# Kernel tuning notes

Hardware: AMD Instinct MI355X
Metric: run time of the kernel (lower is better)

The kernel has to match this reference:

```python
import jax, jax.numpy as jnp
import numpy as np

B, I, H = 2048, 512, 512


def _hamilton_matrix(W):
    """W: [4, O, Iin] quaternion weight components (r,i,j,k).
    Returns real block matrix M: [4*Iin, 4*O] implementing the Hamilton
    product W (*) x for component-major flattened input [r|i|j|k]."""
    Wr, Wi, Wj, Wk = W[0].T, W[1].T, W[2].T, W[3].T  # each [Iin, O]
    row_r = jnp.concatenate([Wr, Wi, Wj, Wk], axis=1)
    row_i = jnp.concatenate([-Wi, Wr, Wk, -Wj], axis=1)
    row_j = jnp.concatenate([-Wj, -Wk, Wr, Wi], axis=1)
    row_k = jnp.concatenate([-Wk, Wj, -Wi, Wr], axis=1)
    return jnp.concatenate([row_r, row_i, row_j, row_k], axis=0)


def qlinear(x, W, b=None):
    """x: [B, Iin, 4]; W: [4, O, Iin]; b: [O, 4] or None -> [B, O, 4]."""
    Bn, Iin, _ = x.shape
    O = W.shape[1]
    xf = x.transpose(0, 2, 1).reshape(Bn, 4 * Iin)  # component-major flatten
    out = xf @ _hamilton_matrix(W)                   # [B, 4*O]
    out = out.reshape(Bn, 4, O).transpose(0, 2, 1)   # [B, O, 4]
    if b is not None:
        out = out + b
    return out


def setup_inputs() -> dict:
    key = jax.random.key(0)
    ks = jax.random.split(key, 16)
    s_in = 0.02   # weight scale for numerical sanity
    d = {
        "x": jax.random.normal(ks[0], (B, I, 4), jnp.float32),
        "h": jax.random.normal(ks[1], (B, H, 4), jnp.float32),
        "c": jax.random.normal(ks[2], (B, H, 4), jnp.float32),
        "Wi_w": jax.random.normal(ks[3], (4, H, I), jnp.float32) * s_in,
        "Wf_w": jax.random.normal(ks[4], (4, H, I), jnp.float32) * s_in,
        "Wo_w": jax.random.normal(ks[5], (4, H, I), jnp.float32) * s_in,
        "Wc_w": jax.random.normal(ks[6], (4, H, I), jnp.float32) * s_in,
        "Ui_w": jax.random.normal(ks[7], (4, H, H), jnp.float32) * s_in,
        "Uf_w": jax.random.normal(ks[8], (4, H, H), jnp.float32) * s_in,
        "Uo_w": jax.random.normal(ks[9], (4, H, H), jnp.float32) * s_in,
        "Uc_w": jax.random.normal(ks[10], (4, H, H), jnp.float32) * s_in,
        "Ui_b": jax.random.normal(ks[11], (H, 4), jnp.float32) * s_in,
        "Uf_b": jax.random.normal(ks[12], (H, 4), jnp.float32) * s_in,
        "Uo_b": jax.random.normal(ks[13], (H, 4), jnp.float32) * s_in,
        "Uc_b": jax.random.normal(ks[14], (H, 4), jnp.float32) * s_in,
    }
    return d


def reference(x, h, c, Wi_w, Wf_w, Wo_w, Wc_w, Ui_w, Uf_w, Uo_w, Uc_w,
              Ui_b, Uf_b, Uo_b, Uc_b):
    # Scalar gates from real (index-0) component of quaternion gate preacts.
    i_pre = qlinear(x, Wi_w) + qlinear(h, Ui_w, Ui_b)
    f_pre = qlinear(x, Wf_w) + qlinear(h, Uf_w, Uf_b)
    o_pre = qlinear(x, Wo_w) + qlinear(h, Uo_w, Uo_b)
    c_tilde = jnp.tanh(qlinear(x, Wc_w) + qlinear(h, Uc_w, Uc_b))
    i = jax.nn.sigmoid(i_pre[..., 0])[..., None]  # [B, H, 1] broadcasts over 4 comps
    f = jax.nn.sigmoid(f_pre[..., 0])[..., None]
    o = jax.nn.sigmoid(o_pre[..., 0])[..., None]
    c_t = f * c + i * c_tilde
    h_t = o * jnp.tanh(c_t)
    return (h_t, c_t)
```

## Files before the change

### kernel.cpp

```cpp
#include <hip/hip_runtime.h>
#include <hip/hip_bf16.h>


#define BDIM 256

typedef __attribute__((ext_vector_type(8))) short short8;
typedef __attribute__((ext_vector_type(4))) float f32x4;

typedef const __attribute__((address_space(1))) void* gptr_t;
typedef __attribute__((address_space(3))) void* lptr_t;

__device__ __forceinline__ ushort f2b(float f) {
  __hip_bfloat16 h = __float2bfloat16(f);
  union { __hip_bfloat16 b; ushort u; } cv;
  cv.b = h;
  return cv.u;
}

__global__ __launch_bounds__(BDIM) void pack_a_kernel(
    const float* __restrict__ x, const float* __restrict__ h,
    ushort* __restrict__ A) {
  int tid = blockIdx.x * BDIM + threadIdx.x;
  int b = tid >> 8;
  int pos0 = (tid & 255) << 2;
  const float* src = (pos0 < 512)
      ? (x + ((size_t)b * 512 + pos0) * 4)
      : (h + ((size_t)b * 512 + (pos0 - 512)) * 4);
  float4 q0 = reinterpret_cast<const float4*>(src)[0];
  float4 q1 = reinterpret_cast<const float4*>(src)[1];
  float4 q2 = reinterpret_cast<const float4*>(src)[2];
  float4 q3 = reinterpret_cast<const float4*>(src)[3];
  ushort* Ab = A + (size_t)b * 4096 + pos0;
  union { ushort u[4]; uint2 v; } r0, r1, r2, r3;
  r0.u[0] = f2b(q0.x); r0.u[1] = f2b(q1.x); r0.u[2] = f2b(q2.x); r0.u[3] = f2b(q3.x);
  r1.u[0] = f2b(q0.y); r1.u[1] = f2b(q1.y); r1.u[2] = f2b(q2.y); r1.u[3] = f2b(q3.y);
  r2.u[0] = f2b(q0.z); r2.u[1] = f2b(q1.z); r2.u[2] = f2b(q2.z); r2.u[3] = f2b(q3.z);
  r3.u[0] = f2b(q0.w); r3.u[1] = f2b(q1.w); r3.u[2] = f2b(q2.w); r3.u[3] = f2b(q3.w);
  *reinterpret_cast<uint2*>(Ab)        = r0.v;
  *reinterpret_cast<uint2*>(Ab + 1024) = r1.v;
  *reinterpret_cast<uint2*>(Ab + 2048) = r2.v;
  *reinterpret_cast<uint2*>(Ab + 3072) = r3.v;
}

__global__ __launch_bounds__(BDIM) void pack_w_kernel(
    const float* __restrict__ w0, const float* __restrict__ w1,
    const float* __restrict__ w2, const float* __restrict__ w3,
    const float* __restrict__ u0, const float* __restrict__ u1,
    const float* __restrict__ u2, const float* __restrict__ u3,
    ushort* __restrict__ Wp) {
  int tid = blockIdx.x * BDIM + threadIdx.x;
  int n = tid >> 9;
  int k = (tid & 511) << 3;
  int blk = n >> 9, o = n & 511;
  int cin = k >> 10, pos = k & 1023;
  int part = pos >> 9, ii = pos & 511;
  int g  = blk < 3 ? blk : 3;
  int co = blk < 3 ? 0 : blk - 3;
  int comp = cin ^ co;
  float sg = ((0x5390u >> ((cin << 2) | co)) & 1u) ? -1.0f : 1.0f;
  const float* base;
  if (part == 0) base = (g == 0) ? w0 : (g == 1) ? w1 : (g == 2) ? w2 : w3;
  else           base = (g == 0) ? u0 : (g == 1) ? u1 : (g == 2) ? u2 : u3;
  const float* p = base + (size_t)comp * 262144 + (size_t)o * 512 + ii;
  float4 v0 = *reinterpret_cast<const float4*>(p);
  float4 v1 = *reinterpret_cast<const float4*>(p + 4);
  union { ushort u[8]; uint4 v; } r;
  r.u[0] = f2b(sg * v0.x); r.u[1] = f2b(sg * v0.y);
  r.u[2] = f2b(sg * v0.z); r.u[3] = f2b(sg * v0.w);
  r.u[4] = f2b(sg * v1.x); r.u[5] = f2b(sg * v1.y);
  r.u[6] = f2b(sg * v1.z); r.u[7] = f2b(sg * v1.w);
  *reinterpret_cast<uint4*>(Wp + (size_t)n * 4096 + k) = r.v;
}

__global__ __launch_bounds__(BDIM, 2) void gemm_kernel(
    const ushort* __restrict__ A, const ushort* __restrict__ Bt,
    float* __restrict__ C) {
  __shared__ ushort As[128 * 32];
  __shared__ ushort Bs[128 * 32];
  const int t = threadIdx.x;
  const int lane = t & 63;
  const int wid = t >> 6;
  const int wm = wid >> 1, wn = wid & 1;
  const int lrow = lane & 15;
  const int lk = (lane >> 4) << 3;
  const int m0 = blockIdx.y * 128;
  const int n0 = blockIdx.x * 128;

  f32x4 acc[4][4];
#pragma unroll
  for (int mi = 0; mi < 4; ++mi)
#pragma unroll
    for (int ni = 0; ni < 4; ++ni)
      acc[mi][ni] = (f32x4){0.f, 0.f, 0.f, 0.f};

  const int rA = t >> 2;
  const int cA = (t & 3) << 3;
  const ushort* Abase = A + (size_t)m0 * 4096;
  const ushort* Bbase = Bt + (size_t)n0 * 4096;

  for (int kt = 0; kt < 4096; kt += 32) {
#pragma unroll
    for (int ch = 0; ch < 2; ++ch) {
      const ushort* ga = Abase + (size_t)(ch * 64 + rA) * 4096 + kt + cA;
      const ushort* gb = Bbase + (size_t)(ch * 64 + rA) * 4096 + kt + cA;
      __builtin_amdgcn_global_load_lds((gptr_t)ga, (lptr_t)(As + ch * 2048 + t * 8),
                                       16, 0, 0);
      __builtin_amdgcn_global_load_lds((gptr_t)gb, (lptr_t)(Bs + ch * 2048 + t * 8),
                                       16, 0, 0);
    }
    __syncthreads();
    short8 a[4], b[4];
#pragma unroll
    for (int f = 0; f < 4; ++f) {
      a[f] = *reinterpret_cast<const short8*>(As + (wm * 64 + f * 16 + lrow) * 32 + lk);
      b[f] = *reinterpret_cast<const short8*>(Bs + (wn * 64 + f * 16 + lrow) * 32 + lk);
    }
#pragma unroll
    for (int mi = 0; mi < 4; ++mi)
#pragma unroll
      for (int ni = 0; ni < 4; ++ni)
        acc[mi][ni] = __builtin_amdgcn_mfma_f32_16x16x32_bf16(
            a[mi], b[ni], acc[mi][ni], 0, 0, 0);
    __syncthreads();
  }

  const int orow = (lane >> 4) << 2;
#pragma unroll
  for (int mi = 0; mi < 4; ++mi) {
#pragma unroll
    for (int ni = 0; ni < 4; ++ni) {
      float* cp = C + (size_t)(m0 + wm * 64 + mi * 16 + orow) * 3584
                  + (n0 + wn * 64 + ni * 16 + (lane & 15));
#pragma unroll
      for (int r = 0; r < 4; ++r)
        cp[(size_t)r * 3584] = acc[mi][ni][r];
    }
  }
}

__global__ __launch_bounds__(BDIM) void cell_kernel(
    const float* __restrict__ pre, const float* __restrict__ cin,
    const float* __restrict__ bi, const float* __restrict__ bfg,
    const float* __restrict__ bo, const float* __restrict__ bc,
    float* __restrict__ out) {
  int tid = blockIdx.x * BDIM + threadIdx.x;
  int o = tid & 511;
  const float* row = pre + (size_t)(tid >> 9) * 3584;
  float4 bcv = *reinterpret_cast<const float4*>(bc + (size_t)o * 4);
  float ip = row[o]        + bi[o << 2];
  float fp = row[512 + o]  + bfg[o << 2];
  float op = row[1024 + o] + bo[o << 2];
  float g0 = tanhf(row[1536 + o] + bcv.x);
  float g1 = tanhf(row[2048 + o] + bcv.y);
  float g2 = tanhf(row[2560 + o] + bcv.z);
  float g3 = tanhf(row[3072 + o] + bcv.w);
  float ig = 1.f / (1.f + expf(-ip));
  float fg = 1.f / (1.f + expf(-fp));
  float og = 1.f / (1.f + expf(-op));
  float4 cv = *reinterpret_cast<const float4*>(cin + (size_t)tid * 4);
  float4 ct, ht;
  ct.x = fg * cv.x + ig * g0;  ht.x = og * tanhf(ct.x);
  ct.y = fg * cv.y + ig * g1;  ht.y = og * tanhf(ct.y);
  ct.z = fg * cv.z + ig * g2;  ht.z = og * tanhf(ct.z);
  ct.w = fg * cv.w + ig * g3;  ht.w = og * tanhf(ct.w);
  *reinterpret_cast<float4*>(out + (size_t)tid * 4) = ht;
  *reinterpret_cast<float4*>(out + 4194304 + (size_t)tid * 4) = ct;
}

extern "C" void kernel_launch(void* const* d_in, const int* in_sizes, int n_in,
                              void* d_out, int out_size, void* d_ws, size_t ws_size,
                              hipStream_t stream) {
  const float* x   = (const float*)d_in[0];
  const float* h   = (const float*)d_in[1];
  const float* c   = (const float*)d_in[2];
  const float* wi  = (const float*)d_in[3];
  const float* wf  = (const float*)d_in[4];
  const float* wo  = (const float*)d_in[5];
  const float* wc  = (const float*)d_in[6];
  const float* ui  = (const float*)d_in[7];
  const float* uf  = (const float*)d_in[8];
  const float* uo  = (const float*)d_in[9];
  const float* uc  = (const float*)d_in[10];
  const float* bi  = (const float*)d_in[11];
  const float* bf_ = (const float*)d_in[12];
  const float* bo  = (const float*)d_in[13];
  const float* bc  = (const float*)d_in[14];
  float* out = (float*)d_out;

  ushort* A  = (ushort*)d_ws;
  ushort* Wp = (ushort*)((char*)d_ws + (size_t)16777216);
  float* pre = (float*)((char*)d_ws + (size_t)16777216 + 29360128);

  hipLaunchKernelGGL(pack_a_kernel, dim3(2048), dim3(BDIM), 0, stream, x, h, A);
  hipLaunchKernelGGL(pack_w_kernel, dim3(7168), dim3(BDIM), 0, stream,
                     wi, wf, wo, wc, ui, uf, uo, uc, Wp);
  hipLaunchKernelGGL(gemm_kernel, dim3(28, 16), dim3(BDIM), 0, stream, A, Wp, pre);
  hipLaunchKernelGGL(cell_kernel, dim3(4096), dim3(BDIM), 0, stream,
                     pre, c, bi, bf_, bo, bc, out);
}
```

Measured before the change: 247.2 us.

## Fuse LSTM cell epilogue into GEMM and merge pack kernels

Merges the activation and weight pack kernels into one launch. It reorders weight columns so each output index owns 8 contiguous columns (7 gates plus one zero pad), which lets the GEMM block compute complete gate sets for 16 outputs. The cell nonlinearity then runs in the GEMM epilogue through a shared-memory staging tile. This removes the round trip of the fp32 preactivation buffer through global memory and two kernel launches. In exchange it adds padding work (3584 to 4096 columns, 32 column blocks instead of 28) and more shared memory per block, which may reduce occupancy.

```diff
diff --git a/kernel.cpp b/kernel.cpp
--- a/kernel.cpp
+++ b/kernel.cpp
@@ -17,66 +17,75 @@
   return cv.u;
 }
 
-__global__ __launch_bounds__(BDIM) void pack_a_kernel(
+__global__ __launch_bounds__(BDIM) void pack_kernel(
     const float* __restrict__ x, const float* __restrict__ h,
-    ushort* __restrict__ A) {
-  int tid = blockIdx.x * BDIM + threadIdx.x;
-  int b = tid >> 8;
-  int pos0 = (tid & 255) << 2;
-  const float* src = (pos0 < 512)
-      ? (x + ((size_t)b * 512 + pos0) * 4)
-      : (h + ((size_t)b * 512 + (pos0 - 512)) * 4);
-  float4 q0 = reinterpret_cast<const float4*>(src)[0];
-  float4 q1 = reinterpret_cast<const float4*>(src)[1];
-  float4 q2 = reinterpret_cast<const float4*>(src)[2];
-  float4 q3 = reinterpret_cast<const float4*>(src)[3];
-  ushort* Ab = A + (size_t)b * 4096 + pos0;
-  union { ushort u[4]; uint2 v; } r0, r1, r2, r3;
-  r0.u[0] = f2b(q0.x); r0.u[1] = f2b(q1.x); r0.u[2] = f2b(q2.x); r0.u[3] = f2b(q3.x);
-  r1.u[0] = f2b(q0.y); r1.u[1] = f2b(q1.y); r1.u[2] = f2b(q2.y); r1.u[3] = f2b(q3.y);
-  r2.u[0] = f2b(q0.z); r2.u[1] = f2b(q1.z); r2.u[2] = f2b(q2.z); r2.u[3] = f2b(q3.z);
-  r3.u[0] = f2b(q0.w); r3.u[1] = f2b(q1.w); r3.u[2] = f2b(q2.w); r3.u[3] = f2b(q3.w);
-  *reinterpret_cast<uint2*>(Ab)        = r0.v;
-  *reinterpret_cast<uint2*>(Ab + 1024) = r1.v;
-  *reinterpret_cast<uint2*>(Ab + 2048) = r2.v;
-  *reinterpret_cast<uint2*>(Ab + 3072) = r3.v;
-}
-
-__global__ __launch_bounds__(BDIM) void pack_w_kernel(
     const float* __restrict__ w0, const float* __restrict__ w1,
     const float* __restrict__ w2, const float* __restrict__ w3,
     const float* __restrict__ u0, const float* __restrict__ u1,
     const float* __restrict__ u2, const float* __restrict__ u3,
-    ushort* __restrict__ Wp) {
-  int tid = blockIdx.x * BDIM + threadIdx.x;
-  int n = tid >> 9;
-  int k = (tid & 511) << 3;
-  int blk = n >> 9, o = n & 511;
-  int cin = k >> 10, pos = k & 1023;
-  int part = pos >> 9, ii = pos & 511;
-  int g  = blk < 3 ? blk : 3;
-  int co = blk < 3 ? 0 : blk - 3;
-  int comp = cin ^ co;
-  float sg = ((0x5390u >> ((cin << 2) | co)) & 1u) ? -1.0f : 1.0f;
-  const float* base;
-  if (part == 0) base = (g == 0) ? w0 : (g == 1) ? w1 : (g == 2) ? w2 : w3;
-  else           base = (g == 0) ? u0 : (g == 1) ? u1 : (g == 2) ? u2 : u3;
-  const float* p = base + (size_t)comp * 262144 + (size_t)o * 512 + ii;
-  float4 v0 = *reinterpret_cast<const float4*>(p);
-  float4 v1 = *reinterpret_cast<const float4*>(p + 4);
-  union { ushort u[8]; uint4 v; } r;
-  r.u[0] = f2b(sg * v0.x); r.u[1] = f2b(sg * v0.y);
-  r.u[2] = f2b(sg * v0.z); r.u[3] = f2b(sg * v0.w);
-  r.u[4] = f2b(sg * v1.x); r.u[5] = f2b(sg * v1.y);
-  r.u[6] = f2b(sg * v1.z); r.u[7] = f2b(sg * v1.w);
-  *reinterpret_cast<uint4*>(Wp + (size_t)n * 4096 + k) = r.v;
-}
-
-__global__ __launch_bounds__(BDIM, 2) void gemm_kernel(
-    const ushort* __restrict__ A, const ushort* __restrict__ Bt,
-    float* __restrict__ C) {
+    ushort* __restrict__ A, ushort* __restrict__ Wp) {
+  if (blockIdx.x < 2048) {
+    int tid = blockIdx.x * BDIM + threadIdx.x;
+    int b = tid >> 8;
+    int pos0 = (tid & 255) << 2;
+    const float* src = (pos0 < 512)
+        ? (x + ((size_t)b * 512 + pos0) * 4)
+        : (h + ((size_t)b * 512 + (pos0 - 512)) * 4);
+    float4 q0 = reinterpret_cast<const float4*>(src)[0];
+    float4 q1 = reinterpret_cast<const float4*>(src)[1];
+    float4 q2 = reinterpret_cast<const float4*>(src)[2];
+    float4 q3 = reinterpret_cast<const float4*>(src)[3];
+    ushort* Ab = A + (size_t)b * 4096 + pos0;
+    union { ushort u[4]; uint2 v; } r0, r1, r2, r3;
+    r0.u[0] = f2b(q0.x); r0.u[1] = f2b(q1.x); r0.u[2] = f2b(q2.x); r0.u[3] = f2b(q3.x);
+    r1.u[0] = f2b(q0.y); r1.u[1] = f2b(q1.y); r1.u[2] = f2b(q2.y); r1.u[3] = f2b(q3.y);
+    r2.u[0] = f2b(q0.z); r2.u[1] = f2b(q1.z); r2.u[2] = f2b(q2.z); r2.u[3] = f2b(q3.z);
+    r3.u[0] = f2b(q0.w); r3.u[1] = f2b(q1.w); r3.u[2] = f2b(q2.w); r3.u[3] = f2b(q3.w);
+    *reinterpret_cast<uint2*>(Ab)        = r0.v;
+    *reinterpret_cast<uint2*>(Ab + 1024) = r1.v;
+    *reinterpret_cast<uint2*>(Ab + 2048) = r2.v;
+    *reinterpret_cast<uint2*>(Ab + 3072) = r3.v;
+  } else {
+    int tid = (blockIdx.x - 2048) * BDIM + threadIdx.x;
+    int n = tid >> 9;
+    int k = (tid & 511) << 3;
+    ushort* dst = Wp + (size_t)n * 4096 + k;
+    int o = n >> 3, g = n & 7;
+    if (g == 7) {
+      uint4 z = {0u, 0u, 0u, 0u};
+      *reinterpret_cast<uint4*>(dst) = z;
+      return;
+    }
+    int cin = k >> 10, pos = k & 1023;
+    int part = pos >> 9, ii = pos & 511;
+    int gi = (g < 3) ? g : 3;
+    int co = (g < 3) ? 0 : g - 3;
+    int comp = cin ^ co;
+    float sg = ((0x5390u >> ((cin << 2) | co)) & 1u) ? -1.0f : 1.0f;
+    const float* base;
+    if (part == 0) base = (gi == 0) ? w0 : (gi == 1) ? w1 : (gi == 2) ? w2 : w3;
+    else           base = (gi == 0) ? u0 : (gi == 1) ? u1 : (gi == 2) ? u2 : u3;
+    const float* p = base + (size_t)comp * 262144 + (size_t)o * 512 + ii;
+    float4 v0 = *reinterpret_cast<const float4*>(p);
+    float4 v1 = *reinterpret_cast<const float4*>(p + 4);
+    union { ushort u[8]; uint4 v; } r;
+    r.u[0] = f2b(sg * v0.x); r.u[1] = f2b(sg * v0.y);
+    r.u[2] = f2b(sg * v0.z); r.u[3] = f2b(sg * v0.w);
+    r.u[4] = f2b(sg * v1.x); r.u[5] = f2b(sg * v1.y);
+    r.u[6] = f2b(sg * v1.z); r.u[7] = f2b(sg * v1.w);
+    *reinterpret_cast<uint4*>(dst) = r.v;
+  }
+}
+
+__global__ __launch_bounds__(BDIM, 2) void gemm_cell_kernel(
+    const ushort* __restrict__ A, const ushort* __restrict__ Wp,
+    const float* __restrict__ cin_, const float* __restrict__ bi,
+    const float* __restrict__ bfg, const float* __restrict__ bo,
+    const float* __restrict__ bc, float* __restrict__ out) {
   __shared__ ushort As[128 * 32];
   __shared__ ushort Bs[128 * 32];
+  __shared__ float  Es[64 * 132];
+
   const int t = threadIdx.x;
   const int lane = t & 63;
   const int wid = t >> 6;
@@ -96,7 +105,7 @@
   const int rA = t >> 2;
   const int cA = (t & 3) << 3;
   const ushort* Abase = A + (size_t)m0 * 4096;
-  const ushort* Bbase = Bt + (size_t)n0 * 4096;
+  const ushort* Bbase = Wp + (size_t)n0 * 4096;
 
   for (int kt = 0; kt < 4096; kt += 32) {
 #pragma unroll
@@ -124,47 +133,52 @@
     __syncthreads();
   }
 
-  const int orow = (lane >> 4) << 2;
-#pragma unroll
-  for (int mi = 0; mi < 4; ++mi) {
-#pragma unroll
-    for (int ni = 0; ni < 4; ++ni) {
-      float* cp = C + (size_t)(m0 + wm * 64 + mi * 16 + orow) * 3584
-                  + (n0 + wn * 64 + ni * 16 + (lane & 15));
-#pragma unroll
-      for (int r = 0; r < 4; ++r)
-        cp[(size_t)r * 3584] = acc[mi][ni][r];
-    }
+  const int o0 = blockIdx.x * 16;
+  const int lr4 = (lane >> 4) << 2;
+
+#pragma unroll
+  for (int ch = 0; ch < 2; ++ch) {
+    if (wm == ch) {
+#pragma unroll
+      for (int mi = 0; mi < 4; ++mi)
+#pragma unroll
+        for (int ni = 0; ni < 4; ++ni) {
+          float* dst = Es + (mi * 16 + lr4) * 132 + wn * 64 + ni * 16 + lrow;
+#pragma unroll
+          for (int r = 0; r < 4; ++r) dst[r * 132] = acc[mi][ni][r];
+        }
+    }
+    __syncthreads();
+#pragma unroll
+    for (int i = 0; i < 4; ++i) {
+      int p = t + i * 256;
+      int bl = p >> 4;
+      int ol = p & 15;
+      const float* e = Es + bl * 132 + ol * 8;
+      int b = m0 + ch * 64 + bl;
+      int o = o0 + ol;
+      float4 bcv = *reinterpret_cast<const float4*>(bc + (size_t)o * 4);
+      float ip = e[0] + bi[o << 2];
+      float fp = e[1] + bfg[o << 2];
+      float op = e[2] + bo[o << 2];
+      float g0 = tanhf(e[3] + bcv.x);
+      float g1 = tanhf(e[4] + bcv.y);
+      float g2 = tanhf(e[5] + bcv.z);
+      float g3 = tanhf(e[6] + bcv.w);
+      float ig = 1.f / (1.f + expf(-ip));
+      float fg = 1.f / (1.f + expf(-fp));
+      float og = 1.f / (1.f + expf(-op));
+      float4 cv = *reinterpret_cast<const float4*>(cin_ + ((size_t)b * 512 + o) * 4);
+      float4 ct, ht;
+      ct.x = fg * cv.x + ig * g0;  ht.x = og * tanhf(ct.x);
+      ct.y = fg * cv.y + ig * g1;  ht.y = og * tanhf(ct.y);
+      ct.z = fg * cv.z + ig * g2;  ht.z = og * tanhf(ct.z);
+      ct.w = fg * cv.w + ig * g3;  ht.w = og * tanhf(ct.w);
+      *reinterpret_cast<float4*>(out + ((size_t)b * 512 + o) * 4) = ht;
+      *reinterpret_cast<float4*>(out + 4194304 + ((size_t)b * 512 + o) * 4) = ct;
+    }
+    __syncthreads();
   }
-}
-
-__global__ __launch_bounds__(BDIM) void cell_kernel(
-    const float* __restrict__ pre, const float* __restrict__ cin,
-    const float* __restrict__ bi, const float* __restrict__ bfg,
-    const float* __restrict__ bo, const float* __restrict__ bc,
-    float* __restrict__ out) {
-  int tid = blockIdx.x * BDIM + threadIdx.x;
-  int o = tid & 511;
-  const float* row = pre + (size_t)(tid >> 9) * 3584;
-  float4 bcv = *reinterpret_cast<const float4*>(bc + (size_t)o * 4);
-  float ip = row[o]        + bi[o << 2];
-  float fp = row[512 + o]  + bfg[o << 2];
-  float op = row[1024 + o] + bo[o << 2];
-  float g0 = tanhf(row[1536 + o] + bcv.x);
-  float g1 = tanhf(row[2048 + o] + bcv.y);
-  float g2 = tanhf(row[2560 + o] + bcv.z);
-  float g3 = tanhf(row[3072 + o] + bcv.w);
-  float ig = 1.f / (1.f + expf(-ip));
-  float fg = 1.f / (1.f + expf(-fp));
-  float og = 1.f / (1.f + expf(-op));
-  float4 cv = *reinterpret_cast<const float4*>(cin + (size_t)tid * 4);
-  float4 ct, ht;
-  ct.x = fg * cv.x + ig * g0;  ht.x = og * tanhf(ct.x);
-  ct.y = fg * cv.y + ig * g1;  ht.y = og * tanhf(ct.y);
-  ct.z = fg * cv.z + ig * g2;  ht.z = og * tanhf(ct.z);
-  ct.w = fg * cv.w + ig * g3;  ht.w = og * tanhf(ct.w);
-  *reinterpret_cast<float4*>(out + (size_t)tid * 4) = ht;
-  *reinterpret_cast<float4*>(out + 4194304 + (size_t)tid * 4) = ct;
 }
 
 extern "C" void kernel_launch(void* const* d_in, const int* in_sizes, int n_in,
@@ -189,12 +203,9 @@
 
   ushort* A  = (ushort*)d_ws;
   ushort* Wp = (ushort*)((char*)d_ws + (size_t)16777216);
-  float* pre = (float*)((char*)d_ws + (size_t)16777216 + 29360128);
-
-  hipLaunchKernelGGL(pack_a_kernel, dim3(2048), dim3(BDIM), 0, stream, x, h, A);
-  hipLaunchKernelGGL(pack_w_kernel, dim3(7168), dim3(BDIM), 0, stream,
-                     wi, wf, wo, wc, ui, uf, uo, uc, Wp);
-  hipLaunchKernelGGL(gemm_kernel, dim3(28, 16), dim3(BDIM), 0, stream, A, Wp, pre);
-  hipLaunchKernelGGL(cell_kernel, dim3(4096), dim3(BDIM), 0, stream,
-                     pre, c, bi, bf_, bo, bc, out);
-}
+
+  hipLaunchKernelGGL(pack_kernel, dim3(10240), dim3(BDIM), 0, stream,
+                     x, h, wi, wf, wo, wc, ui, uf, uo, uc, A, Wp);
+  hipLaunchKernelGGL(gemm_cell_kernel, dim3(32, 16), dim3(BDIM), 0, stream,
+                     A, Wp, c, bi, bf_, bo, bc, out);
+}
```

Measured after the change: 240.5 us. 1.03x faster.
